# Performance work log

Hardware: AMD Instinct MI355X
Metric: run time of the kernel (lower is better)

Reference implementation:

```python
import jax, jax.numpy as jnp
import numpy as np

EPS_Q = 1e-5
EPS_RMS = 1e-6


def _bitlinear(x, w):
    # absmean ternary weight quantization with STE (STE irrelevant for fwd)
    w_scale = jnp.maximum(jnp.mean(jnp.abs(w)), EPS_Q)
    w_q = jnp.clip(jnp.round(w / w_scale), -1.0, 1.0)
    w_q = jax.lax.stop_gradient(w_q - w) + w
    # per-token absmax activation quantization
    x_scale = jnp.maximum(jnp.max(jnp.abs(x), axis=-1, keepdims=True), EPS_Q)
    x_s = x / x_scale
    out = jnp.einsum('bi,oi->bo', x_s, w_q)
    return out * x_scale


def _rmsnorm(x, g):
    rms = jnp.sqrt(jnp.mean(x * x, axis=-1, keepdims=True) + EPS_RMS)
    return x / rms * g


def setup_inputs() -> dict:
    key = jax.random.key(0)
    ks = jax.random.split(key, 6)
    B, IN, H, OUT = 65536, 784, 1024, 10
    return {
        'x': jax.random.normal(ks[0], (B, IN), dtype=jnp.float32),
        'w1': jax.random.normal(ks[1], (H, IN), dtype=jnp.float32) * 0.02,
        'g1': jnp.ones((H,), dtype=jnp.float32),
        'w2': jax.random.normal(ks[2], (H, H), dtype=jnp.float32) * 0.02,
        'g2': jnp.ones((H,), dtype=jnp.float32),
        'w3': jax.random.normal(ks[3], (OUT, H), dtype=jnp.float32) * 0.02,
    }


def reference(x, w1, g1, w2, g2, w3):
    h = _bitlinear(x, w1)
    h = jax.nn.gelu(_rmsnorm(h, g1), approximate=False)
    h = _bitlinear(h, w2)
    h = jax.nn.gelu(_rmsnorm(h, g2), approximate=False)
    return _bitlinear(h, w3)
```

## Files before the change

### kernel.cpp

```cpp
#include <hip/hip_runtime.h>
#include <hip/hip_bf16.h>
#include <stdint.h>


typedef __attribute__((ext_vector_type(8))) short short8;
typedef __attribute__((ext_vector_type(4))) float f32x4;

#define B_TOTAL 65536
#define IN_DIM 784
#define IN_PAD 896
#define H_DIM 1024
#define OUT_DIM 10
#define OUT_PAD 16

__device__ __forceinline__ unsigned short f2bf(float f) {
    union { float f; unsigned u; } c; c.f = f;
    unsigned r = c.u + 0x7FFFu + ((c.u >> 16) & 1u);
    return (unsigned short)(r >> 16);
}
__device__ __forceinline__ float bf2f(unsigned short h) {
    union { unsigned u; float f; } c; c.u = ((unsigned)h) << 16;
    return c.f;
}

__device__ __forceinline__ float gelu_fast(float t) {
    const float z = t * 0.70710678118f;
    const float s = fabsf(z);
    const float tt = 1.0f / (1.0f + 0.3275911f * s);
    const float e = __expf(-s * s);
    float p = fmaf(tt, 1.061405429f, -1.453152027f);
    p = fmaf(tt, p, 1.421413741f);
    p = fmaf(tt, p, -0.284496736f);
    p = fmaf(tt, p, 0.254829592f);
    float erfa = fmaf(-p * tt, e, 1.0f);
    erfa = copysignf(erfa, z);
    return 0.5f * t * (1.0f + erfa);
}

#define GLOAD16(gp, lp)                                                        \
    __builtin_amdgcn_global_load_lds(                                          \
        (const __attribute__((address_space(1))) void*)(gp),                   \
        (__attribute__((address_space(3))) void*)(lp), 16, 0, 0)

__global__ void absum_kernel(const float* __restrict__ w, int n, double* acc) {
    __shared__ float red[4];
    float s = 0.f;
    for (int i = blockIdx.x * blockDim.x + threadIdx.x; i < n; i += gridDim.x * blockDim.x)
        s += fabsf(w[i]);
#pragma unroll
    for (int o = 32; o > 0; o >>= 1) s += __shfl_xor(s, o);
    if ((threadIdx.x & 63) == 0) red[threadIdx.x >> 6] = s;
    __syncthreads();
    if (threadIdx.x == 0) {
        float t = red[0] + red[1] + red[2] + red[3];
        atomicAdd(acc, (double)t);
    }
}

__global__ void quant_kernel(const float* __restrict__ w, unsigned short* __restrict__ wq,
                             int O, int K, int Kp, const double* sum, int n) {
    int k = blockIdx.x * blockDim.x + threadIdx.x;
    int o = blockIdx.y;
    if (k >= Kp) return;
    float scale = fmaxf((float)(*sum / (double)n), 1e-5f);
    float q = 0.f;
    if (o < O && k < K) {
        float r = rintf(w[(size_t)o * K + k] / scale);
        q = fminf(1.f, fmaxf(-1.f, r));
    }
    wq[(size_t)o * Kp + k] = f2bf(q);
}

__global__ __launch_bounds__(256)
void convert_pad(const float* __restrict__ x, unsigned short* __restrict__ xb) {
    const int g = blockIdx.x * 256 + threadIdx.x;
    const int row = g / 112;
    const int c = (g % 112) * 8;
    short8 v = 0;
    if (c < IN_DIM) {
        const float* p = x + (size_t)row * IN_DIM + c;
        float4 f0 = *(const float4*)p;
        float4 f1 = *(const float4*)(p + 4);
        v[0] = (short)f2bf(f0.x); v[1] = (short)f2bf(f0.y);
        v[2] = (short)f2bf(f0.z); v[3] = (short)f2bf(f0.w);
        v[4] = (short)f2bf(f1.x); v[5] = (short)f2bf(f1.y);
        v[6] = (short)f2bf(f1.z); v[7] = (short)f2bf(f1.w);
    }
    *(short8*)(xb + (size_t)row * IN_PAD + c) = v;
}

template<int KP>
__global__ __launch_bounds__(512, 2)
void gemm_bt(const unsigned short* __restrict__ A, const unsigned short* __restrict__ Bq,
             unsigned short* __restrict__ C) {
    constexpr int NT = KP / 64;
    __shared__ __attribute__((aligned(16))) unsigned short LDS[65536];
    const int tid = threadIdx.x;
    const int lane = tid & 63;
    const int w = tid >> 6;
    const int wm = w >> 2, wn = w & 3;
    const int lr = lane & 15, gq = lane >> 4;
    const int gsw8 = (gq ^ ((lr >> 3) << 1)) * 8;
    const int lrO = lr * 32;
    const int bid = blockIdx.x;
    const int xcd = bid & 7, slot = bid >> 3;
    const int nblk = slot & 3;
    const int mblk = xcd * (gridDim.x >> 5) + (slot >> 2);
    const int m0 = mblk * 256, n0 = nblk * 256;
    const int rS = lane >> 2;
    const int cS = ((lane & 3) ^ ((lane >> 5) << 1)) * 8;
    const int stA0 = w;
    const int stA1 = 8 + w;
    const int stB_P1 = (w >> 2) * 8 + (w & 3);
    const int stB_P3 = stB_P1 + 4;

#define STG(gbase, areaS, st)                                                  \
    {   const unsigned short* _g = (gbase) +                                   \
            (size_t)(((st) >> 1) * 16 + rS) * KP + ((st) & 1) * 32 + cS;       \
        GLOAD16(_g, &LDS[(areaS) + (st) * 512]);                               \
        GLOAD16(_g + (size_t)128 * KP, &LDS[(areaS) + (st) * 512 + 8192]); }
#define ABASE(t) (A + (size_t)m0 * KP + (t) * 64)
#define BBASE(t) (Bq + (size_t)n0 * KP + (t) * 64)
#define LD_A(mq)                                                               \
    _Pragma("unroll") for (int mf = 0; mf < 4; ++mf)                           \
    _Pragma("unroll") for (int kk = 0; kk < 2; ++kk)                           \
        af[mf][kk] = *(const short8*)&LDS[curS +                               \
            ((wm * 8 + (mq) * 4 + mf) * 2 + kk) * 512 + lrO + gsw8];
#define LD_B(nq)                                                               \
    _Pragma("unroll") for (int nf = 0; nf < 2; ++nf)                           \
    _Pragma("unroll") for (int kk = 0; kk < 2; ++kk)                           \
        bf[nf][kk] = *(const short8*)&LDS[curS + 16384 +                       \
            ((wn * 4 + (nq) * 2 + nf) * 2 + kk) * 512 + lrO + gsw8];
#define QMM(mq, nq)                                                            \
    _Pragma("unroll") for (int kk = 0; kk < 2; ++kk)                           \
    _Pragma("unroll") for (int mf = 0; mf < 4; ++mf)                           \
    _Pragma("unroll") for (int nf = 0; nf < 2; ++nf)                           \
        acc[(mq) * 4 + mf][(nq) * 2 + nf] =                                    \
            __builtin_amdgcn_mfma_f32_16x16x32_bf16(af[mf][kk], bf[nf][kk],    \
                acc[(mq) * 4 + mf][(nq) * 2 + nf], 0, 0, 0);

    f32x4 acc[8][4] = {};
    short8 af[4][2], bf[2][2];
    STG(ABASE(0), 0, stA0);
    STG(BBASE(0), 16384, stB_P1);
    STG(BBASE(0), 16384, stB_P3);
    STG(ABASE(0), 0, stA1);
    STG(ABASE(1), 32768, stA0);
    STG(BBASE(1), 49152, stB_P3);
    STG(ABASE(1), 32768, stA1);
    asm volatile("s_waitcnt vmcnt(6)" ::: "memory");
#pragma unroll 2
    for (int t = 0; t < NT; ++t) {
        const int curS = (t & 1) * 32768;
        const int nxtS = curS ^ 32768;
        __builtin_amdgcn_s_barrier();
        LD_A(0); LD_B(0);
        __builtin_amdgcn_s_setprio(1); QMM(0, 0); __builtin_amdgcn_s_setprio(0);
        if (t + 1 < NT) STG(BBASE(t + 1), nxtS + 16384, stB_P1);
        __builtin_amdgcn_s_barrier();
        LD_B(1);
        __builtin_amdgcn_s_setprio(1); QMM(0, 1); __builtin_amdgcn_s_setprio(0);
        if (t + 2 < NT) STG(ABASE(t + 2), curS, stA0);
        __builtin_amdgcn_s_barrier();
        LD_A(1);
        __builtin_amdgcn_s_setprio(1); QMM(1, 1); __builtin_amdgcn_s_setprio(0);
        if (t + 2 < NT) STG(BBASE(t + 2), curS + 16384, stB_P3);
        __builtin_amdgcn_s_barrier();
        LD_B(0);
        __builtin_amdgcn_s_setprio(1); QMM(1, 0); __builtin_amdgcn_s_setprio(0);
        if (t + 2 < NT) STG(ABASE(t + 2), curS, stA1);
        if (t < NT - 2) {
            asm volatile("s_waitcnt vmcnt(6)" ::: "memory");
        } else {
            asm volatile("s_waitcnt vmcnt(0)" ::: "memory");
        }
    }
#pragma unroll
    for (int mf = 0; mf < 8; ++mf) {
        const int grow = m0 + wm * 128 + mf * 16 + (lane >> 4) * 4;
#pragma unroll
        for (int nf = 0; nf < 4; ++nf) {
            const int gcol = n0 + wn * 64 + nf * 16 + lr;
            unsigned short* Cp = C + (size_t)grow * H_DIM + gcol;
#pragma unroll
            for (int j = 0; j < 4; ++j) Cp[(size_t)j * H_DIM] = f2bf(acc[mf][nf][j]);
        }
    }
#undef STG
#undef ABASE
#undef BBASE
#undef LD_A
#undef LD_B
#undef QMM
}

__global__ __launch_bounds__(256)
void norm_gelu(const unsigned short* __restrict__ Hp, const float* __restrict__ g,
               unsigned short* __restrict__ U) {
    const int row = blockIdx.x * 4 + (threadIdx.x >> 6);
    const int lane = threadIdx.x & 63;
    const unsigned short* rp = Hp + (size_t)row * H_DIM;
    short8 v0 = *(const short8*)(rp + lane * 8);
    short8 v1 = *(const short8*)(rp + 512 + lane * 8);
    float f[16];
#pragma unroll
    for (int j = 0; j < 8; ++j) {
        f[j] = bf2f((unsigned short)v0[j]);
        f[8 + j] = bf2f((unsigned short)v1[j]);
    }
    float s = 0.f;
#pragma unroll
    for (int j = 0; j < 16; ++j) s += f[j] * f[j];
#pragma unroll
    for (int o = 32; o > 0; o >>= 1) s += __shfl_xor(s, o);
    const float rinv = 1.f / sqrtf(s * (1.f / 1024.f) + 1e-6f);
    float4 ga0 = *(const float4*)(g + lane * 8);
    float4 ga1 = *(const float4*)(g + lane * 8 + 4);
    float4 gb0 = *(const float4*)(g + 512 + lane * 8);
    float4 gb1 = *(const float4*)(g + 512 + lane * 8 + 4);
    float gv[16] = {ga0.x, ga0.y, ga0.z, ga0.w, ga1.x, ga1.y, ga1.z, ga1.w,
                    gb0.x, gb0.y, gb0.z, gb0.w, gb1.x, gb1.y, gb1.z, gb1.w};
    short8 o0, o1;
#pragma unroll
    for (int j = 0; j < 8; ++j) {
        o0[j] = (short)f2bf(gelu_fast(f[j] * rinv * gv[j]));
        o1[j] = (short)f2bf(gelu_fast(f[8 + j] * rinv * gv[8 + j]));
    }
    unsigned short* up = U + (size_t)row * H_DIM;
    *(short8*)(up + lane * 8) = o0;
    *(short8*)(up + 512 + lane * 8) = o1;
}

__global__ __launch_bounds__(256)
void gemm3_kernel(const unsigned short* __restrict__ A, const unsigned short* __restrict__ Bq,
                  float* __restrict__ out) {
    __shared__ unsigned short Bs[16][1032];
    const int tid = threadIdx.x;
    const int lane = tid & 63;
    const int wid = tid >> 6;
    for (int i = tid; i < 2048; i += 256) {
        const int r = i >> 7, cg = i & 127;
        *(short8*)&Bs[r][cg * 8] = *(const short8*)(Bq + (size_t)r * H_DIM + cg * 8);
    }
    __syncthreads();
    const int m0 = blockIdx.x * 128 + wid * 32;
    const int lr = lane & 15;
    const int lk = (lane >> 4) * 8;
    f32x4 acc[2] = {};
#pragma unroll 4
    for (int ks = 0; ks < 32; ++ks) {
        short8 bv = *(const short8*)&Bs[lr][ks * 32 + lk];
#pragma unroll
        for (int m = 0; m < 2; ++m) {
            short8 a = *(const short8*)(A + (size_t)(m0 + m * 16 + lr) * H_DIM + ks * 32 + lk);
            acc[m] = __builtin_amdgcn_mfma_f32_16x16x32_bf16(a, bv, acc[m], 0, 0, 0);
        }
    }
    if (lr < OUT_DIM) {
#pragma unroll
        for (int m = 0; m < 2; ++m)
#pragma unroll
            for (int j = 0; j < 4; ++j) {
                const int grow = m0 + m * 16 + (lane >> 4) * 4 + j;
                out[(size_t)grow * OUT_DIM + lr] = acc[m][j];
            }
    }
}

extern "C" void kernel_launch(void* const* d_in, const int* in_sizes, int n_in,
                              void* d_out, int out_size, void* d_ws, size_t ws_size,
                              hipStream_t stream) {
    (void)in_sizes; (void)n_in; (void)out_size;
    const float* x  = (const float*)d_in[0];
    const float* w1 = (const float*)d_in[1];
    const float* g1 = (const float*)d_in[2];
    const float* w2 = (const float*)d_in[3];
    const float* g2 = (const float*)d_in[4];
    const float* w3 = (const float*)d_in[5];
    float* out = (float*)d_out;

    uint8_t* ws = (uint8_t*)d_ws;
    double* sums = (double*)ws;
    size_t off = 256;
    unsigned short* w1q = (unsigned short*)(ws + off); off += (size_t)H_DIM * IN_PAD * 2;
    unsigned short* w2q = (unsigned short*)(ws + off); off += (size_t)H_DIM * H_DIM * 2;
    unsigned short* w3q = (unsigned short*)(ws + off); off += (size_t)OUT_PAD * H_DIM * 2;

    size_t rem = (ws_size > off) ? ws_size - off : 0;
    int R = B_TOTAL;
    while (R > 2048 && (size_t)2 * R * H_DIM * 2 > rem) R >>= 1;
    unsigned short* bufA = (unsigned short*)(ws + off);
    unsigned short* bufB = bufA + (size_t)R * H_DIM;

    hipMemsetAsync(sums, 0, 3 * sizeof(double), stream);
    absum_kernel<<<128, 256, 0, stream>>>(w1, H_DIM * IN_DIM, sums + 0);
    absum_kernel<<<128, 256, 0, stream>>>(w2, H_DIM * H_DIM, sums + 1);
    absum_kernel<<<128, 256, 0, stream>>>(w3, OUT_DIM * H_DIM, sums + 2);
    quant_kernel<<<dim3((IN_PAD + 255) / 256, H_DIM), 256, 0, stream>>>(
        w1, w1q, H_DIM, IN_DIM, IN_PAD, sums + 0, H_DIM * IN_DIM);
    quant_kernel<<<dim3((H_DIM + 255) / 256, H_DIM), 256, 0, stream>>>(
        w2, w2q, H_DIM, H_DIM, H_DIM, sums + 1, H_DIM * H_DIM);
    quant_kernel<<<dim3((H_DIM + 255) / 256, OUT_PAD), 256, 0, stream>>>(
        w3, w3q, OUT_DIM, H_DIM, H_DIM, sums + 2, OUT_DIM * H_DIM);

    const int nchunk = B_TOTAL / R;
    for (int c = 0; c < nchunk; ++c) {
        const float* xc = x + (size_t)c * R * IN_DIM;
        convert_pad<<<R * 112 / 256, 256, 0, stream>>>(xc, bufB);
        gemm_bt<IN_PAD><<<(R / 256) * 4, 512, 0, stream>>>(bufB, w1q, bufA);
        norm_gelu<<<R / 4, 256, 0, stream>>>(bufA, g1, bufB);
        gemm_bt<H_DIM><<<(R / 256) * 4, 512, 0, stream>>>(bufB, w2q, bufA);
        norm_gelu<<<R / 4, 256, 0, stream>>>(bufA, g2, bufB);
        gemm3_kernel<<<R / 128, 256, 0, stream>>>(bufB, w3q, out + (size_t)c * R * OUT_DIM);
    }
}
```

Baseline: 490.9 us.

## Fuse second norm-GELU with final projection and batch weight-quant launches

Merges the second RMSNorm+GELU pass with the 10-wide output projection, so the normalized activations stay in LDS instead of being written to and reread from global memory. It also collapses the three abs-sum kernels and three quantize kernels into one launch each to cut launch overhead. In exchange each fused block handles only 16 rows, reloads the full w3q tile into LDS per block, and runs the MFMA stage on a single wavefront while the other three sit idle.

```diff
diff --git a/kernel.cpp b/kernel.cpp
--- a/kernel.cpp
+++ b/kernel.cpp
@@ -42,8 +42,12 @@
         (const __attribute__((address_space(1))) void*)(gp),                   \
         (__attribute__((address_space(3))) void*)(lp), 16, 0, 0)
 
-__global__ void absum_kernel(const float* __restrict__ w, int n, double* acc) {
+__global__ void absum3_kernel(const float* __restrict__ w1, const float* __restrict__ w2,
+                              const float* __restrict__ w3, double* acc) {
     __shared__ float red[4];
+    const int which = blockIdx.y;
+    const float* w = (which == 0) ? w1 : (which == 1) ? w2 : w3;
+    const int n = (which == 0) ? H_DIM * IN_DIM : (which == 1) ? H_DIM * H_DIM : OUT_DIM * H_DIM;
     float s = 0.f;
     for (int i = blockIdx.x * blockDim.x + threadIdx.x; i < n; i += gridDim.x * blockDim.x)
         s += fabsf(w[i]);
@@ -53,14 +57,20 @@
     __syncthreads();
     if (threadIdx.x == 0) {
         float t = red[0] + red[1] + red[2] + red[3];
-        atomicAdd(acc, (double)t);
-    }
-}
-
-__global__ void quant_kernel(const float* __restrict__ w, unsigned short* __restrict__ wq,
-                             int O, int K, int Kp, const double* sum, int n) {
-    int k = blockIdx.x * blockDim.x + threadIdx.x;
-    int o = blockIdx.y;
+        atomicAdd(acc + which, (double)t);
+    }
+}
+
+__global__ void quant_all(const float* __restrict__ w1, const float* __restrict__ w2,
+                          const float* __restrict__ w3,
+                          unsigned short* __restrict__ w1q, unsigned short* __restrict__ w2q,
+                          unsigned short* __restrict__ w3q, const double* sums) {
+    const int k = blockIdx.x * blockDim.x + threadIdx.x;
+    const int y = blockIdx.y;
+    const float* w; unsigned short* wq; int o, O, K, Kp, n; const double* sum;
+    if (y < 1024)      { w = w1; wq = w1q; o = y;        O = H_DIM;  K = IN_DIM; Kp = IN_PAD; n = H_DIM * IN_DIM;  sum = sums + 0; }
+    else if (y < 2048) { w = w2; wq = w2q; o = y - 1024; O = H_DIM;  K = H_DIM;  Kp = H_DIM;  n = H_DIM * H_DIM;  sum = sums + 1; }
+    else               { w = w3; wq = w3q; o = y - 2048; O = OUT_DIM; K = H_DIM; Kp = H_DIM;  n = OUT_DIM * H_DIM; sum = sums + 2; }
     if (k >= Kp) return;
     float scale = fmaxf((float)(*sum / (double)n), 1e-5f);
     float q = 0.f;
@@ -232,38 +242,65 @@
 }
 
 __global__ __launch_bounds__(256)
-void gemm3_kernel(const unsigned short* __restrict__ A, const unsigned short* __restrict__ Bq,
-                  float* __restrict__ out) {
-    __shared__ unsigned short Bs[16][1032];
+void norm_gelu_out(const unsigned short* __restrict__ Hp, const float* __restrict__ g,
+                   const unsigned short* __restrict__ w3q, float* __restrict__ out) {
+    __shared__ unsigned short Us[16][1032];
+    __shared__ unsigned short Ws[16][1032];
     const int tid = threadIdx.x;
-    const int lane = tid & 63;
-    const int wid = tid >> 6;
+    const int lane = tid & 63, wid = tid >> 6;
+    const size_t r0 = (size_t)blockIdx.x * 16;
     for (int i = tid; i < 2048; i += 256) {
         const int r = i >> 7, cg = i & 127;
-        *(short8*)&Bs[r][cg * 8] = *(const short8*)(Bq + (size_t)r * H_DIM + cg * 8);
+        *(short8*)&Ws[r][cg * 8] = *(const short8*)(w3q + (size_t)r * H_DIM + cg * 8);
+    }
+    float4 ga0 = *(const float4*)(g + lane * 8);
+    float4 ga1 = *(const float4*)(g + lane * 8 + 4);
+    float4 gb0 = *(const float4*)(g + 512 + lane * 8);
+    float4 gb1 = *(const float4*)(g + 512 + lane * 8 + 4);
+    float gv[16] = {ga0.x, ga0.y, ga0.z, ga0.w, ga1.x, ga1.y, ga1.z, ga1.w,
+                    gb0.x, gb0.y, gb0.z, gb0.w, gb1.x, gb1.y, gb1.z, gb1.w};
+#pragma unroll
+    for (int rr = 0; rr < 4; ++rr) {
+        const int row = wid * 4 + rr;
+        const unsigned short* rp = Hp + (r0 + row) * H_DIM;
+        short8 v0 = *(const short8*)(rp + lane * 8);
+        short8 v1 = *(const short8*)(rp + 512 + lane * 8);
+        float f[16];
+#pragma unroll
+        for (int j = 0; j < 8; ++j) {
+            f[j] = bf2f((unsigned short)v0[j]);
+            f[8 + j] = bf2f((unsigned short)v1[j]);
+        }
+        float s = 0.f;
+#pragma unroll
+        for (int j = 0; j < 16; ++j) s += f[j] * f[j];
+#pragma unroll
+        for (int o = 32; o > 0; o >>= 1) s += __shfl_xor(s, o);
+        const float rinv = 1.f / sqrtf(s * (1.f / 1024.f) + 1e-6f);
+        short8 o0, o1;
+#pragma unroll
+        for (int j = 0; j < 8; ++j) {
+            o0[j] = (short)f2bf(gelu_fast(f[j] * rinv * gv[j]));
+            o1[j] = (short)f2bf(gelu_fast(f[8 + j] * rinv * gv[8 + j]));
+        }
+        *(short8*)&Us[row][lane * 8] = o0;
+        *(short8*)&Us[row][512 + lane * 8] = o1;
     }
     __syncthreads();
-    const int m0 = blockIdx.x * 128 + wid * 32;
-    const int lr = lane & 15;
-    const int lk = (lane >> 4) * 8;
-    f32x4 acc[2] = {};
-#pragma unroll 4
-    for (int ks = 0; ks < 32; ++ks) {
-        short8 bv = *(const short8*)&Bs[lr][ks * 32 + lk];
-#pragma unroll
-        for (int m = 0; m < 2; ++m) {
-            short8 a = *(const short8*)(A + (size_t)(m0 + m * 16 + lr) * H_DIM + ks * 32 + lk);
-            acc[m] = __builtin_amdgcn_mfma_f32_16x16x32_bf16(a, bv, acc[m], 0, 0, 0);
-        }
-    }
-    if (lr < OUT_DIM) {
-#pragma unroll
-        for (int m = 0; m < 2; ++m)
-#pragma unroll
-            for (int j = 0; j < 4; ++j) {
-                const int grow = m0 + m * 16 + (lane >> 4) * 4 + j;
-                out[(size_t)grow * OUT_DIM + lr] = acc[m][j];
-            }
+    if (wid == 0) {
+        const int lr = lane & 15, lk = (lane >> 4) * 8;
+        f32x4 acc = {};
+#pragma unroll
+        for (int ks = 0; ks < 32; ++ks) {
+            short8 a = *(const short8*)&Us[lr][ks * 32 + lk];
+            short8 b = *(const short8*)&Ws[lr][ks * 32 + lk];
+            acc = __builtin_amdgcn_mfma_f32_16x16x32_bf16(a, b, acc, 0, 0, 0);
+        }
+        if (lr < OUT_DIM) {
+#pragma unroll
+            for (int j = 0; j < 4; ++j)
+                out[(r0 + (lane >> 4) * 4 + j) * OUT_DIM + lr] = acc[j];
+        }
     }
 }
 
@@ -293,15 +330,8 @@
     unsigned short* bufB = bufA + (size_t)R * H_DIM;
 
     hipMemsetAsync(sums, 0, 3 * sizeof(double), stream);
-    absum_kernel<<<128, 256, 0, stream>>>(w1, H_DIM * IN_DIM, sums + 0);
-    absum_kernel<<<128, 256, 0, stream>>>(w2, H_DIM * H_DIM, sums + 1);
-    absum_kernel<<<128, 256, 0, stream>>>(w3, OUT_DIM * H_DIM, sums + 2);
-    quant_kernel<<<dim3((IN_PAD + 255) / 256, H_DIM), 256, 0, stream>>>(
-        w1, w1q, H_DIM, IN_DIM, IN_PAD, sums + 0, H_DIM * IN_DIM);
-    quant_kernel<<<dim3((H_DIM + 255) / 256, H_DIM), 256, 0, stream>>>(
-        w2, w2q, H_DIM, H_DIM, H_DIM, sums + 1, H_DIM * H_DIM);
-    quant_kernel<<<dim3((H_DIM + 255) / 256, OUT_PAD), 256, 0, stream>>>(
-        w3, w3q, OUT_DIM, H_DIM, H_DIM, sums + 2, OUT_DIM * H_DIM);
+    absum3_kernel<<<dim3(128, 3), 256, 0, stream>>>(w1, w2, w3, sums);
+    quant_all<<<dim3(4, 2064), 256, 0, stream>>>(w1, w2, w3, w1q, w2q, w3q, sums);
 
     const int nchunk = B_TOTAL / R;
     for (int c = 0; c < nchunk; ++c) {
@@ -310,7 +340,6 @@
         gemm_bt<IN_PAD><<<(R / 256) * 4, 512, 0, stream>>>(bufB, w1q, bufA);
         norm_gelu<<<R / 4, 256, 0, stream>>>(bufA, g1, bufB);
         gemm_bt<H_DIM><<<(R / 256) * 4, 512, 0, stream>>>(bufB, w2q, bufA);
-        norm_gelu<<<R / 4, 256, 0, stream>>>(bufA, g2, bufB);
-        gemm3_kernel<<<R / 128, 256, 0, stream>>>(bufB, w3q, out + (size_t)c * R * OUT_DIM);
-    }
-}
+        norm_gelu_out<<<R / 16, 256, 0, stream>>>(bufA, g2, w3q, out + (size_t)c * R * OUT_DIM);
+    }
+}
```

Result: faster. 463.1 us (-5.7%).
